# Performance work log

Measured on AMD Instinct MI355X. Metric: run time of the kernel, lower is better.

The kernel has to match this reference:

```python
import jax, jax.numpy as jnp
import numpy as np

N_NODES = 50000
N_EDGES = 1600000
E_DIM = 128
N_LAYERS = 3
N_GRAPHS = 32


def setup_inputs() -> dict:
    key = jax.random.key(0)
    ks = jax.random.split(key, 12)
    x = jax.random.normal(ks[0], (N_NODES,), dtype=jnp.float32)
    edge_index = jax.random.randint(ks[1], (2, N_EDGES), 0, N_NODES, dtype=jnp.int32)
    batch = jnp.sort(jax.random.randint(ks[2], (N_NODES,), 0, N_GRAPHS, dtype=jnp.int32))
    s_in = 1.0  # fan_in = 1 for the first linear
    s_e = 1.0 / np.sqrt(E_DIM)
    lin_w = jax.random.normal(ks[3], (1, E_DIM), jnp.float32) * s_in
    lin_b = jax.random.normal(ks[4], (E_DIM,), jnp.float32) * 0.01
    gcn_w = jax.random.normal(ks[5], (N_LAYERS, E_DIM, E_DIM), jnp.float32) * s_e
    gcn_b = jax.random.normal(ks[6], (N_LAYERS, E_DIM), jnp.float32) * 0.01
    r1_w = jax.random.normal(ks[7], (E_DIM, E_DIM), jnp.float32) * s_e
    r1_b = jax.random.normal(ks[8], (E_DIM,), jnp.float32) * 0.01
    r2_w = jax.random.normal(ks[9], (E_DIM, 1), jnp.float32) * s_e
    r2_b = jax.random.normal(ks[10], (1,), jnp.float32) * 0.01
    return {"x": x, "edge_index": edge_index, "batch": batch,
            "lin_w": lin_w, "lin_b": lin_b, "gcn_w": gcn_w, "gcn_b": gcn_b,
            "r1_w": r1_w, "r1_b": r1_b, "r2_w": r2_w, "r2_b": r2_b}


def reference(x, edge_index, batch, lin_w, lin_b, gcn_w, gcn_b, r1_w, r1_b, r2_w, r2_b):
    # input embedding: x.view(-1, 1) @ W + b -> [N, E]
    h = x.reshape(-1, 1) @ lin_w + lin_b

    # GCN normalization (add self-loops, symmetric deg^-1/2 norm) — structure is
    # identical across layers, so compute once.
    loops = jnp.arange(N_NODES, dtype=edge_index.dtype)
    src = jnp.concatenate([edge_index[0], loops])
    dst = jnp.concatenate([edge_index[1], loops])
    deg = jax.ops.segment_sum(jnp.ones(src.shape[0], h.dtype), dst, num_segments=N_NODES)
    dinv = jnp.where(deg > 0, jax.lax.rsqrt(deg), 0.0)
    norm = (dinv[src] * dinv[dst])[:, None]  # [E+N, 1]

    # NOTE: original calls x.relu() without assignment -> no activation (faithful).
    for l in range(N_LAYERS):
        h = h @ gcn_w[l]                                        # [N, E]
        h = jax.ops.segment_sum(h[src] * norm, dst, num_segments=N_NODES) + gcn_b[l]

    # global_add_pool over graphs
    pooled = jax.ops.segment_sum(h, batch, num_segments=N_GRAPHS)  # [G, E]
    hr = jnp.tanh(pooled @ r1_w + r1_b)
    return hr @ r2_w + r2_b  # [G, 1]
```

## Files before the change

### kernel.cpp

```cpp
#include <hip/hip_runtime.h>
#include <hip/hip_bf16.h>
#include <math.h>

#define NGRAPH 32
#define CAP 10240
#define EPT 24
#define EPB (256 * EPT)

__global__ void k_part(const int* __restrict__ src, const int* __restrict__ dst,
                       int* __restrict__ gcursor, unsigned int* __restrict__ packed, int E) {
    __shared__ unsigned int ldsbuf[EPB];
    __shared__ int hist[256], lofs[256], lcur[256], base[256];
    int tid = threadIdx.x;
    int e0 = blockIdx.x * EPB;
    hist[tid] = 0;
    __syncthreads();
    int d[EPT], s[EPT];
#pragma unroll
    for (int c = 0; c < EPT / 4; c++) {
        int e = e0 + c * 1024 + (tid << 2);
        if (e + 3 < E) {
            int4 dv = *(const int4*)&dst[e];
            int4 sv = *(const int4*)&src[e];
            d[4*c+0] = dv.x; d[4*c+1] = dv.y; d[4*c+2] = dv.z; d[4*c+3] = dv.w;
            s[4*c+0] = sv.x; s[4*c+1] = sv.y; s[4*c+2] = sv.z; s[4*c+3] = sv.w;
            atomicAdd(&hist[dv.x >> 8], 1);
            atomicAdd(&hist[dv.y >> 8], 1);
            atomicAdd(&hist[dv.z >> 8], 1);
            atomicAdd(&hist[dv.w >> 8], 1);
        } else {
#pragma unroll
            for (int k = 0; k < 4; k++) {
                int ee = e + k;
                if (ee < E) {
                    d[4*c+k] = dst[ee]; s[4*c+k] = src[ee];
                    atomicAdd(&hist[d[4*c+k] >> 8], 1);
                } else {
                    d[4*c+k] = -1;
                }
            }
        }
    }
    __syncthreads();
    int v = hist[tid];
    lofs[tid] = v;
    __syncthreads();
    for (int off = 1; off < 256; off <<= 1) {
        int t = (tid >= off) ? lofs[tid - off] : 0;
        __syncthreads();
        lofs[tid] += t;
        __syncthreads();
    }
    int total = lofs[255];
    int excl = lofs[tid] - v;
    lofs[tid] = excl;
    lcur[tid] = excl;
    if (v > 0) base[tid] = tid * CAP + atomicAdd(&gcursor[tid], v);
    __syncthreads();
#pragma unroll
    for (int c = 0; c < EPT; c++) {
        int dd = d[c];
        if (dd >= 0) {
            int bk = dd >> 8;
            int slot = atomicAdd(&lcur[bk], 1);
            ldsbuf[slot] = ((unsigned int)bk << 24) | ((unsigned int)s[c] << 8)
                         | (unsigned int)(dd & 255);
        }
    }
    __syncthreads();
    for (int i = tid; i < total; i += 256) {
        unsigned int w = ldsbuf[i];
        int bk = w >> 24;
        packed[base[bk] + (i - lofs[bk])] = w & 0xFFFFFFu;
    }
}

__global__ void k_bucket(const unsigned int* __restrict__ packed, const int* __restrict__ gcursor,
                         const float* __restrict__ x, const int* __restrict__ batch,
                         int* __restrict__ offs, int* __restrict__ deg,
                         float* __restrict__ dinv, float2* __restrict__ q0,
                         float2* __restrict__ q1, float2* __restrict__ q2,
                         unsigned short* __restrict__ csr, float* __restrict__ S, int N) {
    __shared__ int cnt[256], lofs[256], lcur[256];
    __shared__ float cs[NGRAPH];
    int tid = threadIdx.x;
    int b = blockIdx.x;
    int start = b * CAP;
    int end = start + gcursor[b];
    cnt[tid] = 0;
    if (tid < NGRAPH) cs[tid] = 0.f;
    __syncthreads();
    for (int e = start + tid; e < end; e += 256)
        atomicAdd(&cnt[packed[e] & 255], 1);
    __syncthreads();
    int v = cnt[tid];
    int vp = (v + 1) & ~1;
    lofs[tid] = vp;
    __syncthreads();
    for (int off = 1; off < 256; off <<= 1) {
        int t = (tid >= off) ? lofs[tid - off] : 0;
        __syncthreads();
        lofs[tid] += t;
        __syncthreads();
    }
    int excl = lofs[tid] - vp;
    lcur[tid] = excl;
    int node = b * 256 + tid;
    if (node < N) {
        deg[node] = v;
        offs[node] = start + excl;
        float dv = rsqrtf((float)(v + 1));
        dinv[node] = dv;
        q0[node] = make_float2(x[node] * dv, dv);
        atomicAdd(&cs[batch[node]], 1.f);
        if (v & 1) csr[start + excl + v] = (unsigned short)N;
    }
    if (b == 0 && tid == 0) {
        q0[N] = make_float2(0.f, 0.f);
        q1[N] = make_float2(0.f, 0.f);
        q2[N] = make_float2(0.f, 0.f);
    }
    __syncthreads();
    for (int e = start + tid; e < end; e += 256) {
        unsigned int p = packed[e];
        int pos = start + atomicAdd(&lcur[p & 255], 1);
        csr[pos] = (unsigned short)(p >> 8);
    }
    if (tid < NGRAPH && cs[tid] != 0.f) atomicAdd(&S[tid], cs[tid]);
}

template <int WRITE_Q>
__global__ void k_hop(const float2* __restrict__ qin, float2* __restrict__ outv,
                      const unsigned short* __restrict__ csr,
                      const int* __restrict__ offs, const int* __restrict__ deg,
                      const float* __restrict__ dinv, int N) {
    int tid = threadIdx.x;
    int lane = tid & 15;
    int node = blockIdx.x * 16 + (tid >> 4);
    if (node >= N) return;
    int e = offs[node], ne = deg[node];
    float sx = 0.0f, su = 0.0f;
    for (int j = 2 * lane; j < ne; j += 32) {
        ushort2 c = *(const ushort2*)&csr[e + j];
        float2 a = qin[c.x];
        float2 b = qin[c.y];
        sx += a.x + b.x;
        su += a.y + b.y;
    }
#pragma unroll
    for (int m = 8; m > 0; m >>= 1) {
        sx += __shfl_xor(sx, m);
        su += __shfl_xor(su, m);
    }
    if (lane == 0) {
        float2 qs = qin[node];
        float dv = dinv[node];
        float px = dv * (sx + qs.x), pu = dv * (su + qs.y);
        if (WRITE_Q) outv[node] = make_float2(px * dv, pu * dv);
        else         outv[node] = make_float2(px, pu);
    }
}

__global__ __launch_bounds__(1024) void k_chain(
        const float* __restrict__ lin_w, const float* __restrict__ lin_b,
        const float* __restrict__ gcn_w, const float* __restrict__ gcn_b,
        float* __restrict__ chainv) {
    __shared__ float W[128 * 128];
    __shared__ float v4[4 * 128];
    __shared__ float part[4 * 128 * 8];
    int tid = threadIdx.x;
    int j = tid & 127;
    int ch = tid >> 7;
    if (tid < 128) {
        v4[tid]       = lin_w[tid];
        v4[128 + tid] = lin_b[tid];
        v4[256 + tid] = gcn_b[tid];
        v4[384 + tid] = gcn_b[128 + tid];
    }
    for (int l = 0; l < 3; l++) {
        __syncthreads();
        const float4* Wg = (const float4*)(gcn_w + l * 128 * 128);
        float4* Ws = (float4*)W;
#pragma unroll
        for (int i = 0; i < 4; i++) Ws[tid + i * 1024] = Wg[tid + i * 1024];
        __syncthreads();
        float na = 0.f, nb = 0.f, nc = 0.f, nd = 0.f;
#pragma unroll
        for (int kk = 0; kk < 16; kk++) {
            int k = ch * 16 + kk;
            float w = W[k * 128 + j];
            na += v4[k] * w;
            nb += v4[128 + k] * w;
            nc += v4[256 + k] * w;
            nd += v4[384 + k] * w;
        }
        part[(0 * 128 + j) * 8 + ch] = na;
        part[(1 * 128 + j) * 8 + ch] = nb;
        part[(2 * 128 + j) * 8 + ch] = nc;
        part[(3 * 128 + j) * 8 + ch] = nd;
        __syncthreads();
        if (tid < 512) {
            int vec = tid >> 7, jj = tid & 127;
            float s = 0.f;
#pragma unroll
            for (int c = 0; c < 8; c++) s += part[(vec * 128 + jj) * 8 + c];
            if (vec < 2 || (vec == 2 && l >= 1) || (vec == 3 && l >= 2))
                v4[vec * 128 + jj] = s;
        }
    }
    __syncthreads();
    if (tid < 512) chainv[tid] = v4[tid];
}

__global__ __launch_bounds__(256) void k_mlp(
        const float* __restrict__ S, const float* __restrict__ chainv,
        const float2* __restrict__ q1, const float2* __restrict__ q2,
        const float2* __restrict__ p3, const float* __restrict__ dinv,
        const float* __restrict__ gcn_b,
        const float* __restrict__ r1_w, const float* __restrict__ r1_b,
        const float* __restrict__ r2_w, const float* __restrict__ r2_b,
        float* __restrict__ out, int N) {
    __shared__ float rw[128 * 128];
    __shared__ float pl[128], red[128];
    __shared__ float cnts[NGRAPH];
    __shared__ float r4[4 * 128];
    int tid = threadIdx.x;
    int g = blockIdx.x;
    {
        const float4* Rg = (const float4*)r1_w;
        float4* Rs = (float4*)rw;
#pragma unroll
        for (int i = 0; i < 16; i++) Rs[tid + i * 256] = Rg[tid + i * 256];
    }
    if (tid < NGRAPH) cnts[tid] = S[tid];
    __syncthreads();
    int r0 = 0;
    for (int i = 0; i < g; i++) r0 += (int)cnts[i];
    int cnt = (int)cnts[g];
    int r1 = r0 + cnt;
    float su1 = 0.f, su2 = 0.f, su3 = 0.f, sv3 = 0.f;
    for (int n = r0 + tid; n < r1; n += 256) {
        float inv = 1.0f / dinv[n];
        su1 += q1[n].y * inv;
        su2 += q2[n].y * inv;
        float2 p = p3[n];
        su3 += p.y; sv3 += p.x;
    }
#pragma unroll
    for (int m = 32; m > 0; m >>= 1) {
        su1 += __shfl_xor(su1, m);
        su2 += __shfl_xor(su2, m);
        su3 += __shfl_xor(su3, m);
        sv3 += __shfl_xor(sv3, m);
    }
    int wv = tid >> 6;
    if ((tid & 63) == 0) {
        r4[wv] = su1; r4[4 + wv] = su2; r4[8 + wv] = su3; r4[12 + wv] = sv3;
    }
    __syncthreads();
    su1 = r4[0] + r4[1] + r4[2] + r4[3];
    su2 = r4[4] + r4[5] + r4[6] + r4[7];
    su3 = r4[8] + r4[9] + r4[10] + r4[11];
    sv3 = r4[12] + r4[13] + r4[14] + r4[15];
    const float* b3 = gcn_b + 2 * 128;
    if (tid < 128)
        pl[tid] = sv3 * chainv[tid] + su3 * chainv[128 + tid] + su2 * chainv[256 + tid]
                + su1 * chainv[384 + tid] + (float)cnt * b3[tid];
    __syncthreads();
    int j = tid & 127, half = tid >> 7;
    float acc = 0.f;
#pragma unroll
    for (int kk = 0; kk < 64; kk++) {
        int k = half * 64 + kk;
        acc += pl[k] * rw[k * 128 + j];
    }
    r4[half * 128 + j] = acc;
    __syncthreads();
    if (tid < 128) {
        float a = r4[tid] + r4[128 + tid] + r1_b[tid];
        red[tid] = tanhf(a) * r2_w[tid];
    }
    __syncthreads();
    for (int sft = 64; sft > 0; sft >>= 1) {
        if (tid < sft) red[tid] += red[tid + sft];
        __syncthreads();
    }
    if (tid == 0) out[g] = red[0] + r2_b[0];
}

extern "C" void kernel_launch(void* const* d_in, const int* in_sizes, int n_in,
                              void* d_out, int out_size, void* d_ws, size_t ws_size,
                              hipStream_t stream) {
    const float* x     = (const float*)d_in[0];
    const int*   eidx  = (const int*)d_in[1];
    const int*   batch = (const int*)d_in[2];
    const float* lin_w = (const float*)d_in[3];
    const float* lin_b = (const float*)d_in[4];
    const float* gcn_w = (const float*)d_in[5];
    const float* gcn_b = (const float*)d_in[6];
    const float* r1_w  = (const float*)d_in[7];
    const float* r1_b  = (const float*)d_in[8];
    const float* r2_w  = (const float*)d_in[9];
    const float* r2_b  = (const float*)d_in[10];

    const int N = in_sizes[0];
    const int E = in_sizes[1] / 2;
    const int* src = eidx;
    const int* dst = eidx + E;
    const int NB = (N + 255) / 256;

    char* w = (char*)d_ws;
    float2* q0      = (float2*)w; w += (size_t)(N + 2) * 8;
    float2* q1      = (float2*)w; w += (size_t)(N + 2) * 8;
    float2* q2      = (float2*)w; w += (size_t)(N + 2) * 8;
    float2* p3      = (float2*)w; w += (size_t)(N + 2) * 8;
    unsigned int* packed = (unsigned int*)w; w += (size_t)256 * CAP * 4;
    int*    offs    = (int*)w;    w += (size_t)N * 4;
    int*    deg     = (int*)w;    w += (size_t)N * 4;
    float*  dinv    = (float*)w;  w += (size_t)N * 4;
    int*    gcursor = (int*)w;    w += 256 * 4;
    float*  S       = (float*)w;  w += 64 * 4;
    float*  chainv  = (float*)w;  w += 512 * 4;
    unsigned short* csr = (unsigned short*)w; w += (size_t)256 * CAP * 2 + 256;

    hipMemsetAsync(gcursor, 0, 256 * 4 + 64 * 4, stream);

    k_part<<<(E + EPB - 1) / EPB, 256, 0, stream>>>(src, dst, gcursor, packed, E);
    k_bucket<<<NB, 256, 0, stream>>>(packed, gcursor, x, batch, offs, deg, dinv,
                                     q0, q1, q2, csr, S, N);

    int hop_blocks = (N + 15) / 16;
    k_hop<1><<<hop_blocks, 256, 0, stream>>>(q0, q1, csr, offs, deg, dinv, N);
    k_hop<1><<<hop_blocks, 256, 0, stream>>>(q1, q2, csr, offs, deg, dinv, N);
    k_hop<0><<<hop_blocks, 256, 0, stream>>>(q2, p3, csr, offs, deg, dinv, N);

    k_chain<<<1, 1024, 0, stream>>>(lin_w, lin_b, gcn_w, gcn_b, chainv);
    k_mlp<<<NGRAPH, 256, 0, stream>>>(S, chainv, q1, q2, p3, dinv, gcn_b,
                                      r1_w, r1_b, r2_w, r2_b, (float*)d_out, N);
}
```

Before: 160.9 us.

## Fuse chain into partition kernel, fold third hop into pooling MLP

The weight-chain computation now runs as an extra block of the partition kernel, so it no longer needs its own launch. The third propagation hop is dropped and its per-node aggregation is done inside the per-graph MLP kernel while it pools. Other changes: CSR rows are padded to multiples of four so gathers can use ushort4, hop kernels use a fixed grid-stride with 8 lanes per node, the bucket kernel stages packed edges in LDS, and EPT is reduced. Putting the third hop's gather into only 32 blocks risks serialising about 1.6M gathers on few CUs.

```diff
diff --git a/kernel.cpp b/kernel.cpp
--- a/kernel.cpp
+++ b/kernel.cpp
@@ -1,100 +1,148 @@
 #include <hip/hip_runtime.h>
-#include <hip/hip_bf16.h>
 #include <math.h>
 
 #define NGRAPH 32
 #define CAP 10240
-#define EPT 24
+#define EPT 16
 #define EPB (256 * EPT)
-
-__global__ void k_part(const int* __restrict__ src, const int* __restrict__ dst,
-                       int* __restrict__ gcursor, unsigned int* __restrict__ packed, int E) {
-    __shared__ unsigned int ldsbuf[EPB];
-    __shared__ int hist[256], lofs[256], lcur[256], base[256];
+#define BLK 256
+#define HOPGRID 784
+
+__global__ __launch_bounds__(256) void k_part_chain(
+        const int* __restrict__ src, const int* __restrict__ dst,
+        int* __restrict__ gcursor, unsigned int* __restrict__ packed, int E, int nchunk,
+        const float* __restrict__ lin_w, const float* __restrict__ lin_b,
+        const float* __restrict__ gcn_w, const float* __restrict__ gcn_b,
+        float* __restrict__ chainv) {
+    __shared__ union {
+        struct { unsigned int ldsbuf[EPB]; int hist[256], lofs[256], lcur[256], base[256]; } p;
+        struct { float v4[512]; } c;
+    } sm;
     int tid = threadIdx.x;
+
+    if ((int)blockIdx.x == nchunk) {
+        float* v4 = sm.c.v4;
+        int j = tid & 127, gg = tid >> 7;
+        if (tid < 128) {
+            v4[tid]       = lin_w[tid];
+            v4[128 + tid] = lin_b[tid];
+            v4[256 + tid] = gcn_b[tid];
+            v4[384 + tid] = gcn_b[128 + tid];
+        }
+        __syncthreads();
+        for (int l = 0; l < 3; l++) {
+            const float* W = gcn_w + l * 128 * 128;
+            float a0 = 0.f, a1 = 0.f;
+            for (int k0 = 0; k0 < 128; k0 += 16) {
+                float wreg[16];
+#pragma unroll
+                for (int t = 0; t < 16; t++) wreg[t] = W[(k0 + t) * 128 + j];
+#pragma unroll
+                for (int t = 0; t < 16; t++) {
+                    a0 += v4[gg * 128 + k0 + t] * wreg[t];
+                    a1 += v4[(gg + 2) * 128 + k0 + t] * wreg[t];
+                }
+            }
+            __syncthreads();
+            v4[gg * 128 + j] = a0;
+            bool upd = (gg == 0) ? (l >= 1) : (l >= 2);
+            if (upd) v4[(gg + 2) * 128 + j] = a1;
+            __syncthreads();
+        }
+        chainv[tid]       = v4[tid];
+        chainv[256 + tid] = v4[256 + tid];
+        return;
+    }
+
     int e0 = blockIdx.x * EPB;
-    hist[tid] = 0;
-    __syncthreads();
-    int d[EPT], s[EPT];
+    sm.p.hist[tid] = 0;
+    __syncthreads();
+    int d_[EPT], s_[EPT];
 #pragma unroll
     for (int c = 0; c < EPT / 4; c++) {
         int e = e0 + c * 1024 + (tid << 2);
         if (e + 3 < E) {
             int4 dv = *(const int4*)&dst[e];
             int4 sv = *(const int4*)&src[e];
-            d[4*c+0] = dv.x; d[4*c+1] = dv.y; d[4*c+2] = dv.z; d[4*c+3] = dv.w;
-            s[4*c+0] = sv.x; s[4*c+1] = sv.y; s[4*c+2] = sv.z; s[4*c+3] = sv.w;
-            atomicAdd(&hist[dv.x >> 8], 1);
-            atomicAdd(&hist[dv.y >> 8], 1);
-            atomicAdd(&hist[dv.z >> 8], 1);
-            atomicAdd(&hist[dv.w >> 8], 1);
+            d_[4*c+0] = dv.x; d_[4*c+1] = dv.y; d_[4*c+2] = dv.z; d_[4*c+3] = dv.w;
+            s_[4*c+0] = sv.x; s_[4*c+1] = sv.y; s_[4*c+2] = sv.z; s_[4*c+3] = sv.w;
+            atomicAdd(&sm.p.hist[dv.x >> 8], 1);
+            atomicAdd(&sm.p.hist[dv.y >> 8], 1);
+            atomicAdd(&sm.p.hist[dv.z >> 8], 1);
+            atomicAdd(&sm.p.hist[dv.w >> 8], 1);
         } else {
 #pragma unroll
             for (int k = 0; k < 4; k++) {
                 int ee = e + k;
                 if (ee < E) {
-                    d[4*c+k] = dst[ee]; s[4*c+k] = src[ee];
-                    atomicAdd(&hist[d[4*c+k] >> 8], 1);
+                    d_[4*c+k] = dst[ee]; s_[4*c+k] = src[ee];
+                    atomicAdd(&sm.p.hist[d_[4*c+k] >> 8], 1);
                 } else {
-                    d[4*c+k] = -1;
+                    d_[4*c+k] = -1;
                 }
             }
         }
     }
     __syncthreads();
-    int v = hist[tid];
-    lofs[tid] = v;
+    int v = sm.p.hist[tid];
+    sm.p.lofs[tid] = v;
     __syncthreads();
     for (int off = 1; off < 256; off <<= 1) {
-        int t = (tid >= off) ? lofs[tid - off] : 0;
-        __syncthreads();
-        lofs[tid] += t;
-        __syncthreads();
-    }
-    int total = lofs[255];
-    int excl = lofs[tid] - v;
-    lofs[tid] = excl;
-    lcur[tid] = excl;
-    if (v > 0) base[tid] = tid * CAP + atomicAdd(&gcursor[tid], v);
+        int t = (tid >= off) ? sm.p.lofs[tid - off] : 0;
+        __syncthreads();
+        sm.p.lofs[tid] += t;
+        __syncthreads();
+    }
+    int total = sm.p.lofs[255];
+    int excl  = sm.p.lofs[tid] - v;
+    __syncthreads();
+    sm.p.lofs[tid] = excl;
+    sm.p.lcur[tid] = excl;
+    if (v > 0) sm.p.base[tid] = tid * CAP + atomicAdd(&gcursor[tid], v);
     __syncthreads();
 #pragma unroll
     for (int c = 0; c < EPT; c++) {
-        int dd = d[c];
+        int dd = d_[c];
         if (dd >= 0) {
             int bk = dd >> 8;
-            int slot = atomicAdd(&lcur[bk], 1);
-            ldsbuf[slot] = ((unsigned int)bk << 24) | ((unsigned int)s[c] << 8)
-                         | (unsigned int)(dd & 255);
-        }
-    }
-    __syncthreads();
-    for (int i = tid; i < total; i += 256) {
-        unsigned int w = ldsbuf[i];
+            int slot = atomicAdd(&sm.p.lcur[bk], 1);
+            sm.p.ldsbuf[slot] = ((unsigned int)bk << 24) | ((unsigned int)s_[c] << 8)
+                              | (unsigned int)(dd & 255);
+        }
+    }
+    __syncthreads();
+    for (int i = tid; i < total; i += BLK) {
+        unsigned int w = sm.p.ldsbuf[i];
         int bk = w >> 24;
-        packed[base[bk] + (i - lofs[bk])] = w & 0xFFFFFFu;
-    }
-}
-
-__global__ void k_bucket(const unsigned int* __restrict__ packed, const int* __restrict__ gcursor,
-                         const float* __restrict__ x, const int* __restrict__ batch,
-                         int* __restrict__ offs, int* __restrict__ deg,
-                         float* __restrict__ dinv, float2* __restrict__ q0,
-                         float2* __restrict__ q1, float2* __restrict__ q2,
-                         unsigned short* __restrict__ csr, float* __restrict__ S, int N) {
+        packed[sm.p.base[bk] + (i - sm.p.lofs[bk])] = w & 0xFFFFFFu;
+    }
+}
+
+__global__ __launch_bounds__(256) void k_bucket(
+        const unsigned int* __restrict__ packed, const int* __restrict__ gcursor,
+        const float* __restrict__ x, const int* __restrict__ batch,
+        int* __restrict__ offs, int* __restrict__ deg,
+        float* __restrict__ dinv, float2* __restrict__ q0,
+        float2* __restrict__ q1, float2* __restrict__ q2,
+        unsigned short* __restrict__ csr, float* __restrict__ S, int N) {
+    __shared__ unsigned int buf[CAP];
     __shared__ int cnt[256], lofs[256], lcur[256];
     __shared__ float cs[NGRAPH];
     int tid = threadIdx.x;
     int b = blockIdx.x;
     int start = b * CAP;
-    int end = start + gcursor[b];
+    int len = gcursor[b];
     cnt[tid] = 0;
     if (tid < NGRAPH) cs[tid] = 0.f;
     __syncthreads();
-    for (int e = start + tid; e < end; e += 256)
-        atomicAdd(&cnt[packed[e] & 255], 1);
+    for (int e = tid; e < len; e += BLK) {
+        unsigned int w = packed[start + e];
+        buf[e] = w;
+        atomicAdd(&cnt[w & 255], 1);
+    }
     __syncthreads();
     int v = cnt[tid];
-    int vp = (v + 1) & ~1;
+    int vp = (v + 3) & ~3;
     lofs[tid] = vp;
     __syncthreads();
     for (int off = 1; off < 256; off <<= 1) {
@@ -113,7 +161,8 @@
         dinv[node] = dv;
         q0[node] = make_float2(x[node] * dv, dv);
         atomicAdd(&cs[batch[node]], 1.f);
-        if (v & 1) csr[start + excl + v] = (unsigned short)N;
+        for (int p = v; p < vp; p++)
+            csr[start + excl + p] = (unsigned short)N;
     }
     if (b == 0 && tid == 0) {
         q0[N] = make_float2(0.f, 0.f);
@@ -121,102 +170,58 @@
         q2[N] = make_float2(0.f, 0.f);
     }
     __syncthreads();
-    for (int e = start + tid; e < end; e += 256) {
-        unsigned int p = packed[e];
-        int pos = start + atomicAdd(&lcur[p & 255], 1);
-        csr[pos] = (unsigned short)(p >> 8);
+    for (int e = tid; e < len; e += BLK) {
+        unsigned int w = buf[e];
+        int pos = start + atomicAdd(&lcur[w & 255], 1);
+        csr[pos] = (unsigned short)(w >> 8);
     }
     if (tid < NGRAPH && cs[tid] != 0.f) atomicAdd(&S[tid], cs[tid]);
 }
 
 template <int WRITE_Q>
-__global__ void k_hop(const float2* __restrict__ qin, float2* __restrict__ outv,
-                      const unsigned short* __restrict__ csr,
-                      const int* __restrict__ offs, const int* __restrict__ deg,
-                      const float* __restrict__ dinv, int N) {
-    int tid = threadIdx.x;
-    int lane = tid & 15;
-    int node = blockIdx.x * 16 + (tid >> 4);
-    if (node >= N) return;
-    int e = offs[node], ne = deg[node];
-    float sx = 0.0f, su = 0.0f;
-    for (int j = 2 * lane; j < ne; j += 32) {
-        ushort2 c = *(const ushort2*)&csr[e + j];
-        float2 a = qin[c.x];
-        float2 b = qin[c.y];
-        sx += a.x + b.x;
-        su += a.y + b.y;
-    }
-#pragma unroll
-    for (int m = 8; m > 0; m >>= 1) {
-        sx += __shfl_xor(sx, m);
-        su += __shfl_xor(su, m);
-    }
-    if (lane == 0) {
-        float2 qs = qin[node];
-        float dv = dinv[node];
-        float px = dv * (sx + qs.x), pu = dv * (su + qs.y);
-        if (WRITE_Q) outv[node] = make_float2(px * dv, pu * dv);
-        else         outv[node] = make_float2(px, pu);
-    }
-}
-
-__global__ __launch_bounds__(1024) void k_chain(
-        const float* __restrict__ lin_w, const float* __restrict__ lin_b,
-        const float* __restrict__ gcn_w, const float* __restrict__ gcn_b,
-        float* __restrict__ chainv) {
-    __shared__ float W[128 * 128];
-    __shared__ float v4[4 * 128];
-    __shared__ float part[4 * 128 * 8];
-    int tid = threadIdx.x;
-    int j = tid & 127;
-    int ch = tid >> 7;
-    if (tid < 128) {
-        v4[tid]       = lin_w[tid];
-        v4[128 + tid] = lin_b[tid];
-        v4[256 + tid] = gcn_b[tid];
-        v4[384 + tid] = gcn_b[128 + tid];
-    }
-    for (int l = 0; l < 3; l++) {
-        __syncthreads();
-        const float4* Wg = (const float4*)(gcn_w + l * 128 * 128);
-        float4* Ws = (float4*)W;
-#pragma unroll
-        for (int i = 0; i < 4; i++) Ws[tid + i * 1024] = Wg[tid + i * 1024];
-        __syncthreads();
-        float na = 0.f, nb = 0.f, nc = 0.f, nd = 0.f;
-#pragma unroll
-        for (int kk = 0; kk < 16; kk++) {
-            int k = ch * 16 + kk;
-            float w = W[k * 128 + j];
-            na += v4[k] * w;
-            nb += v4[128 + k] * w;
-            nc += v4[256 + k] * w;
-            nd += v4[384 + k] * w;
-        }
-        part[(0 * 128 + j) * 8 + ch] = na;
-        part[(1 * 128 + j) * 8 + ch] = nb;
-        part[(2 * 128 + j) * 8 + ch] = nc;
-        part[(3 * 128 + j) * 8 + ch] = nd;
-        __syncthreads();
-        if (tid < 512) {
-            int vec = tid >> 7, jj = tid & 127;
-            float s = 0.f;
-#pragma unroll
-            for (int c = 0; c < 8; c++) s += part[(vec * 128 + jj) * 8 + c];
-            if (vec < 2 || (vec == 2 && l >= 1) || (vec == 3 && l >= 2))
-                v4[vec * 128 + jj] = s;
-        }
-    }
-    __syncthreads();
-    if (tid < 512) chainv[tid] = v4[tid];
+__global__ __launch_bounds__(256) void k_hop(
+        const float2* __restrict__ qin, float2* __restrict__ outv,
+        const unsigned short* __restrict__ csr,
+        const int* __restrict__ offs, const int* __restrict__ deg,
+        const float* __restrict__ dinv, int N, int ntiles) {
+    int tid  = threadIdx.x;
+    int lane = tid & 7;
+    int sub  = tid >> 3;
+    for (int t = blockIdx.x; t < ntiles; t += gridDim.x) {
+        int node = t * 32 + sub;
+        if (node >= N) continue;
+        int e = offs[node], ne = deg[node];
+        float sx = 0.0f, su = 0.0f;
+        for (int j = 4 * lane; j < ne; j += 32) {
+            ushort4 c = *(const ushort4*)&csr[e + j];
+            float2 a = qin[c.x];
+            float2 b = qin[c.y];
+            float2 c2 = qin[c.z];
+            float2 d2 = qin[c.w];
+            sx += (a.x + b.x) + (c2.x + d2.x);
+            su += (a.y + b.y) + (c2.y + d2.y);
+        }
+#pragma unroll
+        for (int m = 4; m > 0; m >>= 1) {
+            sx += __shfl_xor(sx, m);
+            su += __shfl_xor(su, m);
+        }
+        if (lane == 0) {
+            float2 qs = qin[node];
+            float dv = dinv[node];
+            float px = dv * (sx + qs.x), pu = dv * (su + qs.y);
+            if (WRITE_Q) outv[node] = make_float2(px * dv, pu * dv);
+            else         outv[node] = make_float2(px, pu);
+        }
+    }
 }
 
 __global__ __launch_bounds__(256) void k_mlp(
         const float* __restrict__ S, const float* __restrict__ chainv,
         const float2* __restrict__ q1, const float2* __restrict__ q2,
-        const float2* __restrict__ p3, const float* __restrict__ dinv,
-        const float* __restrict__ gcn_b,
+        const unsigned short* __restrict__ csr,
+        const int* __restrict__ offs, const int* __restrict__ deg,
+        const float* __restrict__ dinv, const float* __restrict__ gcn_b,
         const float* __restrict__ r1_w, const float* __restrict__ r1_b,
         const float* __restrict__ r2_w, const float* __restrict__ r2_b,
         float* __restrict__ out, int N) {
@@ -237,14 +242,27 @@
     int r0 = 0;
     for (int i = 0; i < g; i++) r0 += (int)cnts[i];
     int cnt = (int)cnts[g];
-    int r1 = r0 + cnt;
+    int r1e = r0 + cnt;
     float su1 = 0.f, su2 = 0.f, su3 = 0.f, sv3 = 0.f;
-    for (int n = r0 + tid; n < r1; n += 256) {
-        float inv = 1.0f / dinv[n];
+    for (int n = r0 + tid; n < r1e; n += BLK) {
+        float dv = dinv[n];
+        float inv = 1.0f / dv;
         su1 += q1[n].y * inv;
-        su2 += q2[n].y * inv;
-        float2 p = p3[n];
-        su3 += p.y; sv3 += p.x;
+        float2 q2n = q2[n];
+        su2 += q2n.y * inv;
+        int e = offs[n], ne = deg[n];
+        float sx = q2n.x, su = q2n.y;
+        for (int j = 0; j < ne; j += 4) {
+            ushort4 c = *(const ushort4*)&csr[e + j];
+            float2 a = q2[c.x];
+            float2 b = q2[c.y];
+            float2 c2 = q2[c.z];
+            float2 d2 = q2[c.w];
+            sx += (a.x + b.x) + (c2.x + d2.x);
+            su += (a.y + b.y) + (c2.y + d2.y);
+        }
+        sv3 += dv * sx;
+        su3 += dv * su;
     }
 #pragma unroll
     for (int m = 32; m > 0; m >>= 1) {
@@ -269,7 +287,7 @@
     __syncthreads();
     int j = tid & 127, half = tid >> 7;
     float acc = 0.f;
-#pragma unroll
+#pragma unroll 8
     for (int kk = 0; kk < 64; kk++) {
         int k = half * 64 + kk;
         acc += pl[k] * rw[k * 128 + j];
@@ -313,7 +331,6 @@
     float2* q0      = (float2*)w; w += (size_t)(N + 2) * 8;
     float2* q1      = (float2*)w; w += (size_t)(N + 2) * 8;
     float2* q2      = (float2*)w; w += (size_t)(N + 2) * 8;
-    float2* p3      = (float2*)w; w += (size_t)(N + 2) * 8;
     unsigned int* packed = (unsigned int*)w; w += (size_t)256 * CAP * 4;
     int*    offs    = (int*)w;    w += (size_t)N * 4;
     int*    deg     = (int*)w;    w += (size_t)N * 4;
@@ -325,16 +342,16 @@
 
     hipMemsetAsync(gcursor, 0, 256 * 4 + 64 * 4, stream);
 
-    k_part<<<(E + EPB - 1) / EPB, 256, 0, stream>>>(src, dst, gcursor, packed, E);
+    const int nchunk = (E + EPB - 1) / EPB;
+    k_part_chain<<<nchunk + 1, 256, 0, stream>>>(src, dst, gcursor, packed, E, nchunk,
+                                                 lin_w, lin_b, gcn_w, gcn_b, chainv);
     k_bucket<<<NB, 256, 0, stream>>>(packed, gcursor, x, batch, offs, deg, dinv,
                                      q0, q1, q2, csr, S, N);
 
-    int hop_blocks = (N + 15) / 16;
-    k_hop<1><<<hop_blocks, 256, 0, stream>>>(q0, q1, csr, offs, deg, dinv, N);
-    k_hop<1><<<hop_blocks, 256, 0, stream>>>(q1, q2, csr, offs, deg, dinv, N);
-    k_hop<0><<<hop_blocks, 256, 0, stream>>>(q2, p3, csr, offs, deg, dinv, N);
-
-    k_chain<<<1, 1024, 0, stream>>>(lin_w, lin_b, gcn_w, gcn_b, chainv);
-    k_mlp<<<NGRAPH, 256, 0, stream>>>(S, chainv, q1, q2, p3, dinv, gcn_b,
+    const int ntiles = (N + 31) / 32;
+    k_hop<1><<<HOPGRID, 256, 0, stream>>>(q0, q1, csr, offs, deg, dinv, N, ntiles);
+    k_hop<1><<<HOPGRID, 256, 0, stream>>>(q1, q2, csr, offs, deg, dinv, N, ntiles);
+
+    k_mlp<<<NGRAPH, 256, 0, stream>>>(S, chainv, q1, q2, csr, offs, deg, dinv, gcn_b,
                                       r1_w, r1_b, r2_w, r2_b, (float*)d_out, N);
 }
```

New measurement: 188.4 us. 17.0% more time.
